# Kernel tuning notes

Measured on AMD Instinct MI355X. Metric: run time of the kernel, lower is better.

Reference implementation:

```python
import jax, jax.numpy as jnp
import numpy as np

B, CIN, C, H, W = 4, 256, 128, 64, 64
LN_EPS = 1e-5


def _conv1x1(x, Wk, bk):
    # x: [B, Cin, H, W], Wk: [Cout, Cin] -> [B, Cout, H, W]
    return jnp.einsum('bchw,oc->bohw', x, Wk) + bk[None, :, None, None]


def setup_inputs() -> dict:
    key = jax.random.key(0)
    ks = jax.random.split(key, 11)
    s_in = 1.0 / np.sqrt(CIN)
    s_c = 1.0 / np.sqrt(C)
    return {
        'x': jax.random.normal(ks[0], (B, CIN, H, W), jnp.float32),
        'Wg': jax.random.normal(ks[1], (C, CIN), jnp.float32) * s_in,
        'bg': jax.random.normal(ks[2], (C,), jnp.float32) * s_in,
        'Wt': jax.random.normal(ks[3], (C, CIN), jnp.float32) * s_in,
        'bt': jax.random.normal(ks[4], (C,), jnp.float32) * s_in,
        'Wp': jax.random.normal(ks[5], (C, CIN), jnp.float32) * s_in,
        'bp': jax.random.normal(ks[6], (C,), jnp.float32) * s_in,
        'Wz': jax.random.normal(ks[7], (CIN, C), jnp.float32) * s_c,
        'bz': jax.random.normal(ks[8], (CIN,), jnp.float32) * s_c,
        'gamma': jax.random.normal(ks[9], (CIN, H, W), jnp.float32),
        'beta': jax.random.normal(ks[10], (CIN,), jnp.float32).reshape(CIN, 1, 1) * jnp.ones((CIN, H, W), jnp.float32),
    }


def reference(x, Wg, bg, Wt, bt, Wp, bp, Wz, bz, gamma, beta):
    b, cin, h, w = x.shape
    n = h * w
    # 1x1 conv projections -> flatten spatial
    g = _conv1x1(x, Wg, bg).reshape(b, C, n).transpose(0, 2, 1)      # [B, N, C]
    theta = _conv1x1(x, Wt, bt).reshape(b, C, n).transpose(0, 2, 1)  # [B, N, C]
    phi = _conv1x1(x, Wp, bp).reshape(b, C, n)                        # [B, C, N]
    # embedded-gaussian attention: no scaling, softmax over keys
    f = jnp.einsum('bnc,bcm->bnm', theta, phi)                        # [B, N, N]
    attn = jax.nn.softmax(f, axis=-1)
    y = jnp.einsum('bnm,bmc->bnc', attn, g)                           # [B, N, C]
    y = y.transpose(0, 2, 1).reshape(b, C, h, w)                      # [B, C, H, W]
    # output projection + LayerNorm over [Cin, H, W]
    z = _conv1x1(y, Wz, bz)                                           # [B, Cin, H, W]
    mean = jnp.mean(z, axis=(1, 2, 3), keepdims=True)
    var = jnp.var(z, axis=(1, 2, 3), keepdims=True)
    ln = (z - mean) * jax.lax.rsqrt(var + LN_EPS) * gamma[None] + beta[None]
    return ln + x
```

## Files before the change

kernel.cpp:

```cpp
#include <hip/hip_runtime.h>
#include <hip/hip_bf16.h>


#define BB   4
#define CINC 256
#define CCH  128
#define NS   4096
#define LN_EPS 1e-5f

typedef unsigned short ushort_t;
typedef unsigned int   uint_t;
typedef __bf16 bf16x8 __attribute__((ext_vector_type(8)));
typedef float  f32x4  __attribute__((ext_vector_type(4)));
typedef float  f32x16 __attribute__((ext_vector_type(16)));

typedef const __attribute__((address_space(1))) void* gas_ptr;
typedef __attribute__((address_space(3))) void*       las_ptr;

__device__ __forceinline__ void gload16(const ushort_t* g, ushort_t* l) {
    __builtin_amdgcn_global_load_lds((gas_ptr)g, (las_ptr)l, 16, 0, 0);
}

__device__ __forceinline__ float4 ld4(const float* p) { return *reinterpret_cast<const float4*>(p); }
__device__ __forceinline__ void   st4(float* p, float4 v) { *reinterpret_cast<float4*>(p) = v; }

__device__ __forceinline__ ushort_t f2bf(float f) {
    __hip_bfloat16 h = __float2bfloat16(f);
    return *reinterpret_cast<ushort_t*>(&h);
}
__device__ __forceinline__ float bf2f(ushort_t u) {
    __hip_bfloat16 h = *reinterpret_cast<__hip_bfloat16*>(&u);
    return __bfloat162float(h);
}
__device__ __forceinline__ uint_t pk2(float a, float b) {
    return (uint_t)f2bf(a) | ((uint_t)f2bf(b) << 16);
}

__device__ __forceinline__ void split8(const float* v, uint_t* hw, uint_t* lw) {
#pragma unroll
    for (int jj = 0; jj < 4; ++jj) {
        ushort_t h0 = f2bf(v[2 * jj]);
        ushort_t h1 = f2bf(v[2 * jj + 1]);
        ushort_t e0 = f2bf(v[2 * jj] - bf2f(h0));
        ushort_t e1 = f2bf(v[2 * jj + 1] - bf2f(h1));
        hw[jj] = (uint_t)h0 | ((uint_t)h1 << 16);
        lw[jj] = (uint_t)e0 | ((uint_t)e1 << 16);
    }
}

__global__ __launch_bounds__(256) void split_kernel(
    const float* __restrict__ x,
    ushort_t* __restrict__ xTh, ushort_t* __restrict__ xTl)
{
    __shared__ float T[64 * 68];

    const int tid = threadIdx.x;
    const int n0  = blockIdx.x * 64;
    const int k0  = blockIdx.y * 64;
    const int b   = blockIdx.z;

#pragma unroll
    for (int u = 0; u < 4; ++u) {
        int fi = u * 256 + tid;
        int k  = fi >> 4;
        int c4 = fi & 15;
        float4 v = ld4(&x[(size_t)(b * CINC + k0 + k) * NS + n0 + c4 * 4]);
        T[(c4 * 4 + 0) * 68 + k] = v.x;
        T[(c4 * 4 + 1) * 68 + k] = v.y;
        T[(c4 * 4 + 2) * 68 + k] = v.z;
        T[(c4 * 4 + 3) * 68 + k] = v.w;
    }
    __syncthreads();

#pragma unroll
    for (int u = 0; u < 2; ++u) {
        int fi = u * 256 + tid;
        int n  = fi >> 3;
        int j  = fi & 7;
        float4 a0 = ld4(&T[n * 68 + j * 8]);
        float4 a1 = ld4(&T[n * 68 + j * 8 + 4]);
        float v[8] = {a0.x, a0.y, a0.z, a0.w, a1.x, a1.y, a1.z, a1.w};
        uint_t hw[4], lw[4];
        split8(v, hw, lw);
        size_t base = (size_t)(b * NS + n0 + n) * CINC + k0 + ((j ^ (n & 7)) * 8);
        *reinterpret_cast<uint4*>(&xTh[base]) = make_uint4(hw[0], hw[1], hw[2], hw[3]);
        *reinterpret_cast<uint4*>(&xTl[base]) = make_uint4(lw[0], lw[1], lw[2], lw[3]);
    }
}

__global__ __launch_bounds__(256) void wsplit_kernel(
    const float* __restrict__ Wt, const float* __restrict__ Wp,
    const float* __restrict__ Wg,
    ushort_t* __restrict__ Whs, ushort_t* __restrict__ Wls)
{
    int task = blockIdx.x * 256 + threadIdx.x;
    if (task >= 384 * 32) return;
    int o = task >> 5;
    int j = task & 31;
    int mid = o >> 7;
    int r   = o & 127;
    const float* Wsel = (mid == 0) ? Wt : (mid == 1) ? Wp : Wg;
    float4 a0 = ld4(&Wsel[(size_t)r * CINC + j * 8]);
    float4 a1 = ld4(&Wsel[(size_t)r * CINC + j * 8 + 4]);
    float v[8] = {a0.x, a0.y, a0.z, a0.w, a1.x, a1.y, a1.z, a1.w};
    uint_t hw[4], lw[4];
    split8(v, hw, lw);
    int kb = j >> 3, jj8 = j & 7;
    size_t base = (size_t)o * CINC + kb * 64 + ((jj8 ^ (o & 7)) * 8);
    *reinterpret_cast<uint4*>(&Whs[base]) = make_uint4(hw[0], hw[1], hw[2], hw[3]);
    *reinterpret_cast<uint4*>(&Wls[base]) = make_uint4(lw[0], lw[1], lw[2], lw[3]);
}

__global__ __launch_bounds__(256) void wsplitz_kernel(
    const float* __restrict__ Wz,
    ushort_t* __restrict__ Wzh, ushort_t* __restrict__ Wzl)
{
    int task = blockIdx.x * 256 + threadIdx.x;
    if (task >= 256 * 16) return;
    int o = task >> 4;
    int j = task & 15;
    float4 a0 = ld4(&Wz[(size_t)o * CCH + j * 8]);
    float4 a1 = ld4(&Wz[(size_t)o * CCH + j * 8 + 4]);
    float v[8] = {a0.x, a0.y, a0.z, a0.w, a1.x, a1.y, a1.z, a1.w};
    uint_t hw[4], lw[4];
    split8(v, hw, lw);
    size_t base = (size_t)o * CCH + (j >> 3) * 64 + (((j & 7) ^ (o & 7)) * 8);
    *reinterpret_cast<uint4*>(&Wzh[base]) = make_uint4(hw[0], hw[1], hw[2], hw[3]);
    *reinterpret_cast<uint4*>(&Wzl[base]) = make_uint4(lw[0], lw[1], lw[2], lw[3]);
}

__global__ __launch_bounds__(256) void proj_mfma_kernel(
    const ushort_t* __restrict__ xTh, const ushort_t* __restrict__ xTl,
    const ushort_t* __restrict__ Whs, const ushort_t* __restrict__ Wls,
    const float* __restrict__ bt, const float* __restrict__ bp,
    const float* __restrict__ bg,
    ushort_t* __restrict__ Qhi, ushort_t* __restrict__ Qlo,
    ushort_t* __restrict__ KhiS, ushort_t* __restrict__ KloS,
    ushort_t* __restrict__ VtS)
{
    __shared__ __align__(16) char smem[65536];
    ushort_t* Wh_l = (ushort_t*)smem;
    ushort_t* Wl_l = (ushort_t*)(smem + 16384);
    ushort_t* Xh_l = (ushort_t*)(smem + 32768);
    ushort_t* Xl_l = (ushort_t*)(smem + 49152);
    float*    T    = (float*)smem;

    const int tid  = threadIdx.x;
    const int w    = tid >> 6;
    const int lane = tid & 63;
    const int l31  = lane & 31;
    const int h    = lane >> 5;
    const int n0   = blockIdx.x * 128;
    const int og   = blockIdx.y;
    const int b    = blockIdx.z;

    const float* bsel = (og == 0) ? bt : (og == 1) ? bp : bg;

    f32x16 acc[4];
#pragma unroll
    for (int ng = 0; ng < 4; ++ng)
#pragma unroll
        for (int r = 0; r < 16; ++r) acc[ng][r] = 0.f;

    const int ol   = w * 32 + l31;
    const int swzq = l31 & 7;

    for (int kb = 0; kb < 4; ++kb) {
        if (kb > 0) __syncthreads();
#pragma unroll
        for (int p = 0; p < 4; ++p) {
            int e  = p * 2048 + tid * 8;
            int rr = e >> 6;
            int kk = e & 63;
            gload16(Whs + (size_t)(og * 128 + rr) * CINC + kb * 64 + kk, Wh_l + e);
            gload16(Wls + (size_t)(og * 128 + rr) * CINC + kb * 64 + kk, Wl_l + e);
            gload16(xTh + (size_t)(b * NS + n0 + rr) * CINC + kb * 64 + kk, Xh_l + e);
            gload16(xTl + (size_t)(b * NS + n0 + rr) * CINC + kb * 64 + kk, Xl_l + e);
        }
        __syncthreads();

        __builtin_amdgcn_s_setprio(1);
#pragma unroll
        for (int k16 = 0; k16 < 4; ++k16) {
            int c8  = k16 * 2 + h;
            int swz = c8 ^ swzq;
            bf16x8 ah = *reinterpret_cast<const bf16x8*>(&Wh_l[ol * 64 + swz * 8]);
            bf16x8 al = *reinterpret_cast<const bf16x8*>(&Wl_l[ol * 64 + swz * 8]);
#pragma unroll
            for (int ng = 0; ng < 4; ++ng) {
                int nl = ng * 32 + l31;
                bf16x8 xh = *reinterpret_cast<const bf16x8*>(&Xh_l[nl * 64 + swz * 8]);
                bf16x8 xl = *reinterpret_cast<const bf16x8*>(&Xl_l[nl * 64 + swz * 8]);
                acc[ng] = __builtin_amdgcn_mfma_f32_32x32x16_bf16(ah, xh, acc[ng], 0, 0, 0);
                acc[ng] = __builtin_amdgcn_mfma_f32_32x32x16_bf16(ah, xl, acc[ng], 0, 0, 0);
                acc[ng] = __builtin_amdgcn_mfma_f32_32x32x16_bf16(al, xh, acc[ng], 0, 0, 0);
            }
        }
        __builtin_amdgcn_s_setprio(0);
    }

    float bv[16];
#pragma unroll
    for (int r = 0; r < 16; ++r)
        bv[r] = bsel[w * 32 + (r & 3) + 8 * (r >> 2) + 4 * h];

    __syncthreads();

    if (og < 2) {
        ushort_t* H = (og == 0) ? Qhi : KhiS;
        ushort_t* L = (og == 0) ? Qlo : KloS;
#pragma unroll
        for (int pass = 0; pass < 2; ++pass) {
#pragma unroll
            for (int ngh = 0; ngh < 2; ++ngh) {
                int ng = pass * 2 + ngh;
                int nl = ngh * 32 + l31;
#pragma unroll
                for (int r = 0; r < 16; ++r) {
                    int o_in = w * 32 + (r & 3) + 8 * (r >> 2) + 4 * h;
                    T[nl * 132 + o_in] = acc[ng][r] + bv[r];
                }
            }
            __syncthreads();
#pragma unroll
            for (int u = 0; u < 4; ++u) {
                int fi = u * 256 + tid;
                int n  = fi >> 4;
                int j  = fi & 15;
                float4 a0 = ld4(&T[n * 132 + j * 8]);
                float4 a1 = ld4(&T[n * 132 + j * 8 + 4]);
                float v[8] = {a0.x, a0.y, a0.z, a0.w, a1.x, a1.y, a1.z, a1.w};
                uint_t hw[4], lw[4];
                split8(v, hw, lw);
                int n_glob = n0 + pass * 64 + n;
                int idx = (og == 1) ? ((j & 8) | ((j & 7) ^ (n & 7))) : j;
                size_t base = (size_t)(b * NS + n_glob) * CCH + idx * 8;
                *reinterpret_cast<uint4*>(&H[base]) = make_uint4(hw[0], hw[1], hw[2], hw[3]);
                *reinterpret_cast<uint4*>(&L[base]) = make_uint4(lw[0], lw[1], lw[2], lw[3]);
            }
            __syncthreads();
        }
    } else {
#pragma unroll
        for (int pass = 0; pass < 2; ++pass) {
            if ((w >> 1) == pass) {
#pragma unroll
                for (int ng = 0; ng < 4; ++ng) {
                    int nl = ng * 32 + l31;
#pragma unroll
                    for (int r = 0; r < 16; ++r) {
                        int c_loc = (w & 1) * 32 + (r & 3) + 8 * (r >> 2) + 4 * h;
                        T[c_loc * 132 + nl] = acc[ng][r] + bv[r];
                    }
                }
            }
            __syncthreads();
#pragma unroll
            for (int u = 0; u < 4; ++u) {
                int fi = u * 256 + tid;
                int c_loc = fi >> 4;
                int nj    = fi & 15;
                float4 a0 = ld4(&T[c_loc * 132 + nj * 8]);
                float4 a1 = ld4(&T[c_loc * 132 + nj * 8 + 4]);
                int c = pass * 64 + c_loc;
                uint4 wv;
                wv.x = pk2(a0.x, a0.y);
                wv.y = pk2(a0.z, a0.w);
                wv.z = pk2(a1.x, a1.y);
                wv.w = pk2(a1.z, a1.w);
                size_t base = (size_t)(b * CCH + c) * NS + n0 + (nj >> 3) * 64
                            + (((nj & 7) ^ (c & 7)) * 8);
                *reinterpret_cast<uint4*>(&VtS[base]) = wv;
            }
            __syncthreads();
        }
    }
}

__global__ __launch_bounds__(256, 2) void attn_kernel(
    const ushort_t* __restrict__ Qhi, const ushort_t* __restrict__ Qlo,
    const ushort_t* __restrict__ KhiS, const ushort_t* __restrict__ KloS,
    const ushort_t* __restrict__ VtS, float* __restrict__ Yp,
    float* __restrict__ ML, int NT)
{
    __shared__ __align__(16) char smem[81920];

    const int tid  = threadIdx.x;
    const int w    = tid >> 6;
    const int lane = tid & 63;
    const int l31  = lane & 31;
    const int h    = lane >> 5;

    int qx, sp, b;
    {
        int lin = (blockIdx.z * gridDim.y + blockIdx.y) * gridDim.x + blockIdx.x;
        if (gridDim.x * gridDim.y * gridDim.z == 512) {
            int xcd  = lin & 7;
            int idx  = lin >> 3;
            int pair = xcd * 2 + (idx >> 5);
            qx = idx & 31;
            b  = pair >> 2;
            sp = pair & 3;
        } else {
            qx = blockIdx.x;
            sp = blockIdx.y;
            b  = blockIdx.z;
        }
    }
    const int n0 = qx * 128;

    bf16x8 qh[8], ql[8];
    {
        const ushort_t* qrh = Qhi + (size_t)(b * NS + n0 + w * 32 + l31) * CCH;
        const ushort_t* qrl = Qlo + (size_t)(b * NS + n0 + w * 32 + l31) * CCH;
#pragma unroll
        for (int cst = 0; cst < 8; ++cst) {
            qh[cst] = *reinterpret_cast<const bf16x8*>(qrh + cst * 16 + h * 8);
            ql[cst] = *reinterpret_cast<const bf16x8*>(qrl + cst * 16 + h * 8);
        }
    }

    f32x16 yacc[4];
#pragma unroll
    for (int cb = 0; cb < 4; ++cb)
#pragma unroll
        for (int r = 0; r < 16; ++r) yacc[cb][r] = 0.f;
    float m_run = -1e30f, l_run = 0.f;

    const ushort_t* Khg = KhiS + (size_t)b * NS * CCH;
    const ushort_t* Klg = KloS + (size_t)b * NS * CCH;
    const ushort_t* Vtg = VtS + (size_t)b * CCH * NS;

    const int ktbase = sp * NT;

    auto gload_k = [&](int ktg, int bi) {
        ushort_t* kh = (ushort_t*)(smem + bi * 16384);
        ushort_t* kl = (ushort_t*)(smem + 32768 + bi * 16384);
        const size_t koff = (size_t)ktg * 8192;
#pragma unroll
        for (int i = 0; i < 4; ++i) {
            int off = i * 2048 + tid * 8;
            gload16(Khg + koff + off, kh + off);
            gload16(Klg + koff + off, kl + off);
        }
    };
    auto gload_v = [&](int ktg) {
        ushort_t* vb = (ushort_t*)(smem + 65536);
        const int m0 = ktg * 64;
#pragma unroll
        for (int i = 0; i < 4; ++i) {
            int off = i * 2048 + tid * 8;
            int cr = off >> 6;
            int cw = off & 63;
            gload16(Vtg + (size_t)cr * NS + m0 + cw, vb + off);
        }
    };

    gload_k(ktbase, 0);
    __syncthreads();

    const int swzq = l31 & 7;

    for (int kt = 0; kt < NT; ++kt) {
        const int cur = kt & 1;
        const bool more = (kt + 1 < NT);

        gload_v(ktbase + kt);
        if (more) gload_k(ktbase + kt + 1, cur ^ 1);

        const ushort_t* Kh = (const ushort_t*)(smem + cur * 16384);
        const ushort_t* Kl = (const ushort_t*)(smem + 32768 + cur * 16384);

        f32x16 sacc[2];
#pragma unroll
        for (int k2 = 0; k2 < 2; ++k2)
#pragma unroll
            for (int r = 0; r < 16; ++r) sacc[k2][r] = 0.f;

        __builtin_amdgcn_s_setprio(1);
#pragma unroll
        for (int cst = 0; cst < 8; ++cst) {
            int cc  = cst * 2 + h;
            int swz = (cc & 8) | ((cc & 7) ^ swzq);
#pragma unroll
            for (int k2 = 0; k2 < 2; ++k2) {
                int addr = (k2 * 32 + l31) * 128 + swz * 8;
                bf16x8 ah = *reinterpret_cast<const bf16x8*>(&Kh[addr]);
                bf16x8 al = *reinterpret_cast<const bf16x8*>(&Kl[addr]);
                sacc[k2] = __builtin_amdgcn_mfma_f32_32x32x16_bf16(ah, qh[cst], sacc[k2], 0, 0, 0);
                sacc[k2] = __builtin_amdgcn_mfma_f32_32x32x16_bf16(al, qh[cst], sacc[k2], 0, 0, 0);
                sacc[k2] = __builtin_amdgcn_mfma_f32_32x32x16_bf16(ah, ql[cst], sacc[k2], 0, 0, 0);
            }
        }
        __builtin_amdgcn_s_setprio(0);

        float mx = sacc[0][0];
#pragma unroll
        for (int r = 1; r < 16; ++r) mx = fmaxf(mx, sacc[0][r]);
#pragma unroll
        for (int r = 0; r < 16; ++r) mx = fmaxf(mx, sacc[1][r]);
        mx = fmaxf(mx, __shfl_xor(mx, 32));

        const bool defer = __all(mx - m_run <= 8.0f);
        float mref, alpha;
        if (defer) { mref = m_run; alpha = 1.0f; }
        else       { mref = fmaxf(m_run, mx); alpha = __expf(m_run - mref); }

        bf16x8 pb[4];
        float psum = 0.f;
#pragma unroll
        for (int k2 = 0; k2 < 2; ++k2) {
            float pe[16];
#pragma unroll
            for (int r = 0; r < 16; ++r) {
                pe[r] = __expf(sacc[k2][r] - mref);
                psum += pe[r];
            }
#pragma unroll
            for (int a = 0; a < 2; ++a) {
                uint_t w0 = pk2(pe[8 * a + 0], pe[8 * a + 1]);
                uint_t w1 = pk2(pe[8 * a + 2], pe[8 * a + 3]);
                uint_t w2 = pk2(pe[8 * a + 4], pe[8 * a + 5]);
                uint_t w3 = pk2(pe[8 * a + 6], pe[8 * a + 7]);
                uint_t s0 = (uint_t)__shfl_xor((int)w0, 32);
                uint_t s1 = (uint_t)__shfl_xor((int)w1, 32);
                uint_t s2 = (uint_t)__shfl_xor((int)w2, 32);
                uint_t s3 = (uint_t)__shfl_xor((int)w3, 32);
                uint_t u0 = h ? s2 : w0;
                uint_t u1 = h ? s3 : w1;
                uint_t u2 = h ? w2 : s0;
                uint_t u3 = h ? w3 : s1;
                uint4 packed = make_uint4(u0, u1, u2, u3);
                pb[k2 * 2 + a] = *reinterpret_cast<bf16x8*>(&packed);
            }
        }
        psum += __shfl_xor(psum, 32);

        if (more) {
            asm volatile("s_waitcnt vmcnt(8)" ::: "memory");
        } else {
            asm volatile("s_waitcnt vmcnt(0)" ::: "memory");
        }
        __builtin_amdgcn_s_barrier();
        __builtin_amdgcn_sched_barrier(0);

        if (defer) {
            l_run += psum;
        } else {
            l_run = l_run * alpha + psum;
            m_run = mref;
#pragma unroll
            for (int cb = 0; cb < 4; ++cb)
#pragma unroll
                for (int r = 0; r < 16; ++r) yacc[cb][r] *= alpha;
        }

        const ushort_t* Vl = (const ushort_t*)(smem + 65536);
        __builtin_amdgcn_s_setprio(1);
#pragma unroll
        for (int cb = 0; cb < 4; ++cb) {
            int crow = (cb * 32 + l31) * 64;
#pragma unroll
            for (int ks = 0; ks < 4; ++ks) {
                int kc = ks * 2 + h;
                bf16x8 av = *reinterpret_cast<const bf16x8*>(&Vl[crow + (kc ^ swzq) * 8]);
                yacc[cb] = __builtin_amdgcn_mfma_f32_32x32x16_bf16(av, pb[ks], yacc[cb], 0, 0, 0);
            }
        }
        __builtin_amdgcn_s_setprio(0);

        __syncthreads();
    }

    float* stage = (float*)smem;
    float* Ybase = Yp + ((size_t)(sp * BB + b) * NS + n0) * CCH;
#pragma unroll
    for (int pass = 0; pass < 2; ++pass) {
        if ((w >> 1) == pass) {
            int qrow = (w & 1) * 32 + l31;
#pragma unroll
            for (int cb = 0; cb < 4; ++cb)
#pragma unroll
                for (int r = 0; r < 16; ++r) {
                    int c = cb * 32 + (r & 3) + 8 * (r >> 2) + 4 * h;
                    stage[qrow * 132 + c] = yacc[cb][r];
                }
        }
        __syncthreads();
#pragma unroll
        for (int u = 0; u < 8; ++u) {
            int idx = u * 256 + tid;
            int row = idx >> 5;
            int c4  = idx & 31;
            st4(&Ybase[(size_t)(pass * 64 + row) * CCH + c4 * 4],
                ld4(&stage[row * 132 + c4 * 4]));
        }
        __syncthreads();
    }
    if (h == 0) {
        size_t mi = ((size_t)(sp * BB + b) * NS + n0 + w * 32 + l31) * 2;
        ML[mi + 0] = m_run;
        ML[mi + 1] = l_run;
    }
}

__global__ __launch_bounds__(256) void merge_kernel(
    const float* __restrict__ Yp, const float* __restrict__ ML,
    ushort_t* __restrict__ Ymh, ushort_t* __restrict__ Yml, int nsplit)
{
    const int total = BB * NS * (CCH / 8);
    for (int t = blockIdx.x * 256 + threadIdx.x; t < total;
         t += gridDim.x * 256) {
        int b = t >> 16;
        int r = t & 65535;
        int n = r >> 4;
        int j = r & 15;

        float ms[4], ls[4];
        float m = -1e30f;
#pragma unroll
        for (int s = 0; s < 4; ++s) {
            if (s < nsplit) {
                size_t mi = ((size_t)(s * BB + b) * NS + n) * 2;
                ms[s] = ML[mi + 0];
                ls[s] = ML[mi + 1];
                m = fmaxf(m, ms[s]);
            }
        }
        float den = 0.f;
        float wt[4];
#pragma unroll
        for (int s = 0; s < 4; ++s) {
            if (s < nsplit) {
                wt[s] = __expf(ms[s] - m);
                den += ls[s] * wt[s];
            }
        }
        float inv = 1.0f / den;

        float acc[8] = {0.f, 0.f, 0.f, 0.f, 0.f, 0.f, 0.f, 0.f};
#pragma unroll
        for (int s = 0; s < 4; ++s) {
            if (s < nsplit) {
                float a = wt[s] * inv;
                const float* yr = &Yp[((size_t)(s * BB + b) * NS + n) * CCH + j * 8];
                float4 y0 = ld4(yr);
                float4 y1 = ld4(yr + 4);
                acc[0] += a * y0.x; acc[1] += a * y0.y;
                acc[2] += a * y0.z; acc[3] += a * y0.w;
                acc[4] += a * y1.x; acc[5] += a * y1.y;
                acc[6] += a * y1.z; acc[7] += a * y1.w;
            }
        }
        uint_t hw[4], lw[4];
        split8(acc, hw, lw);
        size_t base = (size_t)(b * NS + n) * CCH + (j >> 3) * 64
                    + (((j & 7) ^ (n & 7)) * 8);
        *reinterpret_cast<uint4*>(&Ymh[base]) = make_uint4(hw[0], hw[1], hw[2], hw[3]);
        *reinterpret_cast<uint4*>(&Yml[base]) = make_uint4(lw[0], lw[1], lw[2], lw[3]);
    }
}

__global__ __launch_bounds__(256) void zgemm_kernel(
    const ushort_t* __restrict__ Ymh, const ushort_t* __restrict__ Yml,
    const ushort_t* __restrict__ Wzh, const ushort_t* __restrict__ Wzl,
    const float* __restrict__ bz, float* __restrict__ Z,
    float* __restrict__ partials)
{
    __shared__ __align__(16) char smem[65536];
    ushort_t* Wh_l = (ushort_t*)smem;
    ushort_t* Wl_l = (ushort_t*)(smem + 16384);
    ushort_t* Yh_l = (ushort_t*)(smem + 32768);
    ushort_t* Yl_l = (ushort_t*)(smem + 49152);
    __shared__ float red[8];

    const int tid  = threadIdx.x;
    const int w    = tid >> 6;
    const int lane = tid & 63;
    const int l31  = lane & 31;
    const int h    = lane >> 5;
    const int n0   = blockIdx.x * 128;
    const int o0   = blockIdx.y * 128;
    const int b    = blockIdx.z;

    f32x16 acc[4];
#pragma unroll
    for (int ng = 0; ng < 4; ++ng)
#pragma unroll
        for (int r = 0; r < 16; ++r) acc[ng][r] = 0.f;

    const int ol   = w * 32 + l31;
    const int swzq = l31 & 7;

    for (int kb = 0; kb < 2; ++kb) {
        if (kb > 0) __syncthreads();
#pragma unroll
        for (int p = 0; p < 4; ++p) {
            int e  = p * 2048 + tid * 8;
            int rr = e >> 6;
            int kk = e & 63;
            gload16(Wzh + (size_t)(o0 + rr) * CCH + kb * 64 + kk, Wh_l + e);
            gload16(Wzl + (size_t)(o0 + rr) * CCH + kb * 64 + kk, Wl_l + e);
            gload16(Ymh + (size_t)(b * NS + n0 + rr) * CCH + kb * 64 + kk, Yh_l + e);
            gload16(Yml + (size_t)(b * NS + n0 + rr) * CCH + kb * 64 + kk, Yl_l + e);
        }
        __syncthreads();

        __builtin_amdgcn_s_setprio(1);
#pragma unroll
        for (int k16 = 0; k16 < 4; ++k16) {
            int c8  = k16 * 2 + h;
            int swz = c8 ^ swzq;
            bf16x8 ah = *reinterpret_cast<const bf16x8*>(&Wh_l[ol * 64 + swz * 8]);
            bf16x8 al = *reinterpret_cast<const bf16x8*>(&Wl_l[ol * 64 + swz * 8]);
#pragma unroll
            for (int ng = 0; ng < 4; ++ng) {
                int nl = ng * 32 + l31;
                bf16x8 yh = *reinterpret_cast<const bf16x8*>(&Yh_l[nl * 64 + swz * 8]);
                bf16x8 yl = *reinterpret_cast<const bf16x8*>(&Yl_l[nl * 64 + swz * 8]);
                acc[ng] = __builtin_amdgcn_mfma_f32_32x32x16_bf16(ah, yh, acc[ng], 0, 0, 0);
                acc[ng] = __builtin_amdgcn_mfma_f32_32x32x16_bf16(ah, yl, acc[ng], 0, 0, 0);
                acc[ng] = __builtin_amdgcn_mfma_f32_32x32x16_bf16(al, yh, acc[ng], 0, 0, 0);
            }
        }
        __builtin_amdgcn_s_setprio(0);
    }

    float s = 0.f, s2 = 0.f;
#pragma unroll
    for (int r = 0; r < 16; ++r) {
        int o = o0 + w * 32 + (r & 3) + 8 * (r >> 2) + 4 * h;
        float bias = bz[o];
        float* zrow = &Z[(size_t)(b * CINC + o) * NS + n0 + l31];
#pragma unroll
        for (int ng = 0; ng < 4; ++ng) {
            float v = acc[ng][r] + bias;
            zrow[ng * 32] = v;
            s  += v;
            s2 += v * v;
        }
    }
#pragma unroll
    for (int off = 1; off < 64; off <<= 1) {
        s  += __shfl_xor(s, off);
        s2 += __shfl_xor(s2, off);
    }
    if (lane == 0) { red[w * 2] = s; red[w * 2 + 1] = s2; }
    __syncthreads();
    if (tid == 0) {
        float ts  = red[0] + red[2] + red[4] + red[6];
        float ts2 = red[1] + red[3] + red[5] + red[7];
        int pidx = (b * 2 + blockIdx.y) * 32 + blockIdx.x;
        partials[pidx * 2 + 0] = ts;
        partials[pidx * 2 + 1] = ts2;
    }
}

__global__ void ln_stats_kernel(const float* __restrict__ partials,
                                float* __restrict__ stats)
{
    const int b = blockIdx.x;
    const int t = threadIdx.x;
    float s  = partials[(size_t)(b * 64 + t) * 2 + 0];
    float s2 = partials[(size_t)(b * 64 + t) * 2 + 1];
#pragma unroll
    for (int off = 1; off < 64; off <<= 1) {
        s  += __shfl_xor(s, off);
        s2 += __shfl_xor(s2, off);
    }
    if (t == 0) {
        const float M = 1048576.f;
        float mean = s / M;
        float var  = s2 / M - mean * mean;
        stats[b * 2 + 0] = mean;
        stats[b * 2 + 1] = rsqrtf(var + LN_EPS);
    }
}

__global__ __launch_bounds__(256) void final_kernel(
    const float* __restrict__ Z, const float* __restrict__ x,
    const float* __restrict__ gamma, const float* __restrict__ beta,
    const float* __restrict__ stats, float* __restrict__ out)
{
    const int total4 = BB * CINC * NS / 4;
    for (int i4 = blockIdx.x * 256 + threadIdx.x; i4 < total4;
         i4 += gridDim.x * 256) {
        int b  = i4 >> 18;
        int r4 = i4 & ((1 << 18) - 1);
        float mean = stats[b * 2 + 0];
        float rstd = stats[b * 2 + 1];
        float4 zv = ld4(&Z[(size_t)i4 * 4]);
        float4 xv = ld4(&x[(size_t)i4 * 4]);
        float4 gv = ld4(&gamma[(size_t)r4 * 4]);
        float4 bv = ld4(&beta[(size_t)r4 * 4]);
        float4 o;
        o.x = (zv.x - mean) * rstd * gv.x + bv.x + xv.x;
        o.y = (zv.y - mean) * rstd * gv.y + bv.y + xv.y;
        o.z = (zv.z - mean) * rstd * gv.z + bv.z + xv.z;
        o.w = (zv.w - mean) * rstd * gv.w + bv.w + xv.w;
        st4(&out[(size_t)i4 * 4], o);
    }
}

extern "C" void kernel_launch(void* const* d_in, const int* in_sizes, int n_in,
                              void* d_out, int out_size, void* d_ws, size_t ws_size,
                              hipStream_t stream)
{
    const float* x     = (const float*)d_in[0];
    const float* Wg    = (const float*)d_in[1];
    const float* bg    = (const float*)d_in[2];
    const float* Wt    = (const float*)d_in[3];
    const float* bt    = (const float*)d_in[4];
    const float* Wp    = (const float*)d_in[5];
    const float* bp    = (const float*)d_in[6];
    const float* Wz    = (const float*)d_in[7];
    const float* bz    = (const float*)d_in[8];
    const float* gamma = (const float*)d_in[9];
    const float* beta  = (const float*)d_in[10];
    float* out = (float*)d_out;

    const size_t SZH = (size_t)BB * NS * CCH * sizeof(ushort_t);
    const size_t need4 = 5 * SZH
                       + (size_t)4 * BB * NS * CCH * sizeof(float)
                       + (size_t)4 * BB * NS * 2 * sizeof(float)
                       + (size_t)BB * 64 * 2 * sizeof(float) + 256;
    const int nsplit = (ws_size >= need4) ? 4 : 2;
    const int NT = (NS / 64) / nsplit;

    char* p = (char*)d_ws;
    ushort_t* Qhi  = (ushort_t*)p; p += SZH;
    ushort_t* Qlo  = (ushort_t*)p; p += SZH;
    ushort_t* KhiS = (ushort_t*)p; p += SZH;
    ushort_t* KloS = (ushort_t*)p; p += SZH;
    ushort_t* VtS  = (ushort_t*)p; p += SZH;
    float* Yp = (float*)p; p += (size_t)nsplit * BB * NS * CCH * sizeof(float);
    float* ML = (float*)p; p += (size_t)nsplit * BB * NS * 2 * sizeof(float);
    float* partials = (float*)p; p += BB * 64 * 2 * sizeof(float);
    float* stats    = (float*)p;

    ushort_t* Ymh = (ushort_t*)Qhi;
    ushort_t* Yml = (ushort_t*)Qlo;
    ushort_t* Wzh = (ushort_t*)KhiS;
    ushort_t* Wzl = (ushort_t*)KloS;
    float*    Z   = (float*)Yp;

    ushort_t* xTh = (ushort_t*)Yp;
    ushort_t* xTl = xTh + (size_t)BB * NS * CINC;
    ushort_t* Whs = (ushort_t*)((char*)Yp + 2 * (size_t)BB * NS * CINC * 2);
    ushort_t* Wls = Whs + (size_t)384 * CINC;

    split_kernel<<<dim3(NS / 64, CINC / 64, BB), 256, 0, stream>>>(x, xTh, xTl);
    wsplit_kernel<<<dim3(48), 256, 0, stream>>>(Wt, Wp, Wg, Whs, Wls);
    proj_mfma_kernel<<<dim3(NS / 128, 3, BB), 256, 0, stream>>>(
        xTh, xTl, Whs, Wls, bt, bp, bg, Qhi, Qlo, KhiS, KloS, VtS);
    attn_kernel<<<dim3(NS / 128, nsplit, BB), 256, 0, stream>>>(
        Qhi, Qlo, KhiS, KloS, VtS, Yp, ML, NT);
    wsplitz_kernel<<<dim3(16), 256, 0, stream>>>(Wz, Wzh, Wzl);
    merge_kernel<<<dim3(1024), 256, 0, stream>>>(Yp, ML, Ymh, Yml, nsplit);
    zgemm_kernel<<<dim3(NS / 128, 2, BB), 256, 0, stream>>>(
        Ymh, Yml, Wzh, Wzl, bz, Z, partials);
    ln_stats_kernel<<<dim3(BB), 64, 0, stream>>>(partials, stats);
    final_kernel<<<dim3(2048), 256, 0, stream>>>(Z, x, gamma, beta, stats, out);
}
```

Baseline: 135.7 us.

## Software-pipeline attention loop with 32-key tiles, overlapping QK of next tile with PV

Shrinks the key tile from 64 to 32 keys and restructures the attention loop so the QK^T MFMAs for tile kt run alongside softmax and PV for tile kt-1. V is now double-buffered with K, and the V transposed layout swizzle is changed to match 32-wide rows. LDS use drops from 80KB to 48KB, which may allow more resident blocks, but the loop runs twice as many iterations with extra barriers and finer-grained waits.

```diff
diff --git a/kernel.cpp b/kernel.cpp
--- a/kernel.cpp
+++ b/kernel.cpp
@@ -268,8 +268,8 @@
                 wv.y = pk2(a0.z, a0.w);
                 wv.z = pk2(a1.x, a1.y);
                 wv.w = pk2(a1.z, a1.w);
-                size_t base = (size_t)(b * CCH + c) * NS + n0 + (nj >> 3) * 64
-                            + (((nj & 7) ^ (c & 7)) * 8);
+                size_t base = (size_t)(b * CCH + c) * NS + n0 + (nj >> 2) * 32
+                            + (((nj & 3) ^ (c & 3)) * 8);
                 *reinterpret_cast<uint4*>(&VtS[base]) = wv;
             }
             __syncthreads();
@@ -283,7 +283,7 @@
     const ushort_t* __restrict__ VtS, float* __restrict__ Yp,
     float* __restrict__ ML, int NT)
 {
-    __shared__ __align__(16) char smem[81920];
+    __shared__ __align__(16) char smem[49152];
 
     const int tid  = threadIdx.x;
     const int w    = tid >> 6;
@@ -302,9 +302,7 @@
             b  = pair >> 2;
             sp = pair & 3;
         } else {
-            qx = blockIdx.x;
-            sp = blockIdx.y;
-            b  = blockIdx.z;
+            qx = blockIdx.x; sp = blockIdx.y; b = blockIdx.z;
         }
     }
     const int n0 = qx * 128;
@@ -326,124 +324,89 @@
 #pragma unroll
         for (int r = 0; r < 16; ++r) yacc[cb][r] = 0.f;
     float m_run = -1e30f, l_run = 0.f;
+    f32x16 sC, sP;
+    bf16x8 pb[2];
 
     const ushort_t* Khg = KhiS + (size_t)b * NS * CCH;
     const ushort_t* Klg = KloS + (size_t)b * NS * CCH;
     const ushort_t* Vtg = VtS + (size_t)b * CCH * NS;
 
     const int ktbase = sp * NT;
+    const int swzq = l31 & 7;
+    const int swzv = l31 & 3;
 
     auto gload_k = [&](int ktg, int bi) {
-        ushort_t* kh = (ushort_t*)(smem + bi * 16384);
-        ushort_t* kl = (ushort_t*)(smem + 32768 + bi * 16384);
-        const size_t koff = (size_t)ktg * 8192;
-#pragma unroll
-        for (int i = 0; i < 4; ++i) {
+        ushort_t* kh = (ushort_t*)(smem + bi * 8192);
+        ushort_t* kl = (ushort_t*)(smem + 16384 + bi * 8192);
+        const size_t koff = (size_t)ktg * 4096;
+#pragma unroll
+        for (int i = 0; i < 2; ++i) {
             int off = i * 2048 + tid * 8;
             gload16(Khg + koff + off, kh + off);
             gload16(Klg + koff + off, kl + off);
         }
     };
-    auto gload_v = [&](int ktg) {
-        ushort_t* vb = (ushort_t*)(smem + 65536);
-        const int m0 = ktg * 64;
-#pragma unroll
-        for (int i = 0; i < 4; ++i) {
+    auto gload_v = [&](int ktg, int bi) {
+        ushort_t* vb = (ushort_t*)(smem + 32768 + bi * 8192);
+        const int m0 = ktg * 32;
+#pragma unroll
+        for (int i = 0; i < 2; ++i) {
             int off = i * 2048 + tid * 8;
-            int cr = off >> 6;
-            int cw = off & 63;
+            int cr = off >> 5;
+            int cw = off & 31;
             gload16(Vtg + (size_t)cr * NS + m0 + cw, vb + off);
         }
     };
 
-    gload_k(ktbase, 0);
-    __syncthreads();
-
-    const int swzq = l31 & 7;
-
-    for (int kt = 0; kt < NT; ++kt) {
-        const int cur = kt & 1;
-        const bool more = (kt + 1 < NT);
-
-        gload_v(ktbase + kt);
-        if (more) gload_k(ktbase + kt + 1, cur ^ 1);
-
-        const ushort_t* Kh = (const ushort_t*)(smem + cur * 16384);
-        const ushort_t* Kl = (const ushort_t*)(smem + 32768 + cur * 16384);
-
-        f32x16 sacc[2];
-#pragma unroll
-        for (int k2 = 0; k2 < 2; ++k2)
-#pragma unroll
-            for (int r = 0; r < 16; ++r) sacc[k2][r] = 0.f;
-
+    auto qk = [&](int bi, f32x16& s) {
+        const ushort_t* Kh = (const ushort_t*)(smem + bi * 8192);
+        const ushort_t* Kl = (const ushort_t*)(smem + 16384 + bi * 8192);
         __builtin_amdgcn_s_setprio(1);
 #pragma unroll
         for (int cst = 0; cst < 8; ++cst) {
             int cc  = cst * 2 + h;
             int swz = (cc & 8) | ((cc & 7) ^ swzq);
-#pragma unroll
-            for (int k2 = 0; k2 < 2; ++k2) {
-                int addr = (k2 * 32 + l31) * 128 + swz * 8;
-                bf16x8 ah = *reinterpret_cast<const bf16x8*>(&Kh[addr]);
-                bf16x8 al = *reinterpret_cast<const bf16x8*>(&Kl[addr]);
-                sacc[k2] = __builtin_amdgcn_mfma_f32_32x32x16_bf16(ah, qh[cst], sacc[k2], 0, 0, 0);
-                sacc[k2] = __builtin_amdgcn_mfma_f32_32x32x16_bf16(al, qh[cst], sacc[k2], 0, 0, 0);
-                sacc[k2] = __builtin_amdgcn_mfma_f32_32x32x16_bf16(ah, ql[cst], sacc[k2], 0, 0, 0);
-            }
+            int addr = l31 * 128 + swz * 8;
+            bf16x8 ah = *reinterpret_cast<const bf16x8*>(&Kh[addr]);
+            bf16x8 al = *reinterpret_cast<const bf16x8*>(&Kl[addr]);
+            s = __builtin_amdgcn_mfma_f32_32x32x16_bf16(ah, qh[cst], s, 0, 0, 0);
+            s = __builtin_amdgcn_mfma_f32_32x32x16_bf16(al, qh[cst], s, 0, 0, 0);
+            s = __builtin_amdgcn_mfma_f32_32x32x16_bf16(ah, ql[cst], s, 0, 0, 0);
         }
         __builtin_amdgcn_s_setprio(0);
-
-        float mx = sacc[0][0];
-#pragma unroll
-        for (int r = 1; r < 16; ++r) mx = fmaxf(mx, sacc[0][r]);
-#pragma unroll
-        for (int r = 0; r < 16; ++r) mx = fmaxf(mx, sacc[1][r]);
+    };
+
+    auto softmax_pack = [&](f32x16& s) {
+        float mx = s[0];
+#pragma unroll
+        for (int r = 1; r < 16; ++r) mx = fmaxf(mx, s[r]);
         mx = fmaxf(mx, __shfl_xor(mx, 32));
-
         const bool defer = __all(mx - m_run <= 8.0f);
         float mref, alpha;
         if (defer) { mref = m_run; alpha = 1.0f; }
         else       { mref = fmaxf(m_run, mx); alpha = __expf(m_run - mref); }
-
-        bf16x8 pb[4];
         float psum = 0.f;
 #pragma unroll
-        for (int k2 = 0; k2 < 2; ++k2) {
-            float pe[16];
-#pragma unroll
-            for (int r = 0; r < 16; ++r) {
-                pe[r] = __expf(sacc[k2][r] - mref);
-                psum += pe[r];
-            }
-#pragma unroll
-            for (int a = 0; a < 2; ++a) {
-                uint_t w0 = pk2(pe[8 * a + 0], pe[8 * a + 1]);
-                uint_t w1 = pk2(pe[8 * a + 2], pe[8 * a + 3]);
-                uint_t w2 = pk2(pe[8 * a + 4], pe[8 * a + 5]);
-                uint_t w3 = pk2(pe[8 * a + 6], pe[8 * a + 7]);
-                uint_t s0 = (uint_t)__shfl_xor((int)w0, 32);
-                uint_t s1 = (uint_t)__shfl_xor((int)w1, 32);
-                uint_t s2 = (uint_t)__shfl_xor((int)w2, 32);
-                uint_t s3 = (uint_t)__shfl_xor((int)w3, 32);
-                uint_t u0 = h ? s2 : w0;
-                uint_t u1 = h ? s3 : w1;
-                uint_t u2 = h ? w2 : s0;
-                uint_t u3 = h ? w3 : s1;
-                uint4 packed = make_uint4(u0, u1, u2, u3);
-                pb[k2 * 2 + a] = *reinterpret_cast<bf16x8*>(&packed);
-            }
+        for (int r = 0; r < 16; ++r) {
+            float v = __expf(s[r] - mref);
+            s[r] = v;
+            psum += v;
+        }
+#pragma unroll
+        for (int a = 0; a < 2; ++a) {
+            uint_t w0 = pk2(s[8 * a + 0], s[8 * a + 1]);
+            uint_t w1 = pk2(s[8 * a + 2], s[8 * a + 3]);
+            uint_t w2 = pk2(s[8 * a + 4], s[8 * a + 5]);
+            uint_t w3 = pk2(s[8 * a + 6], s[8 * a + 7]);
+            uint_t s0 = (uint_t)__shfl_xor((int)w0, 32);
+            uint_t s1 = (uint_t)__shfl_xor((int)w1, 32);
+            uint_t s2 = (uint_t)__shfl_xor((int)w2, 32);
+            uint_t s3 = (uint_t)__shfl_xor((int)w3, 32);
+            uint4 packed = make_uint4(h ? s2 : w0, h ? s3 : w1,
+                                      h ? w2 : s0, h ? w3 : s1);
+            pb[a] = *reinterpret_cast<bf16x8*>(&packed);
         }
         psum += __shfl_xor(psum, 32);
-
-        if (more) {
-            asm volatile("s_waitcnt vmcnt(8)" ::: "memory");
-        } else {
-            asm volatile("s_waitcnt vmcnt(0)" ::: "memory");
-        }
-        __builtin_amdgcn_s_barrier();
-        __builtin_amdgcn_sched_barrier(0);
-
         if (defer) {
             l_run += psum;
         } else {
@@ -454,23 +417,65 @@
 #pragma unroll
                 for (int r = 0; r < 16; ++r) yacc[cb][r] *= alpha;
         }
-
-        const ushort_t* Vl = (const ushort_t*)(smem + 65536);
+    };
+
+    auto pv = [&](int bi) {
+        const ushort_t* Vl = (const ushort_t*)(smem + 32768 + bi * 8192);
         __builtin_amdgcn_s_setprio(1);
 #pragma unroll
         for (int cb = 0; cb < 4; ++cb) {
-            int crow = (cb * 32 + l31) * 64;
-#pragma unroll
-            for (int ks = 0; ks < 4; ++ks) {
+            int crow = (cb * 32 + l31) * 32;
+#pragma unroll
+            for (int ks = 0; ks < 2; ++ks) {
                 int kc = ks * 2 + h;
-                bf16x8 av = *reinterpret_cast<const bf16x8*>(&Vl[crow + (kc ^ swzq) * 8]);
+                bf16x8 av = *reinterpret_cast<const bf16x8*>(&Vl[crow + (kc ^ swzv) * 8]);
                 yacc[cb] = __builtin_amdgcn_mfma_f32_32x32x16_bf16(av, pb[ks], yacc[cb], 0, 0, 0);
             }
         }
         __builtin_amdgcn_s_setprio(0);
-
-        __syncthreads();
-    }
+    };
+
+    gload_k(ktbase, 0);
+    __syncthreads();
+    gload_k(ktbase + 1, 1);
+    gload_v(ktbase, 0);
+#pragma unroll
+    for (int r = 0; r < 16; ++r) sC[r] = 0.f;
+    qk(0, sC);
+    asm volatile("s_waitcnt vmcnt(2)\ns_barrier" ::: "memory");
+    __builtin_amdgcn_sched_barrier(0);
+    sP = sC;
+
+    for (int kt = 1; kt < NT; ++kt) {
+        const int cur = kt & 1;
+        if (kt + 1 < NT) gload_k(ktbase + kt + 1, cur ^ 1);
+        gload_v(ktbase + kt, cur);
+
+#pragma unroll
+        for (int r = 0; r < 16; ++r) sC[r] = 0.f;
+        qk(cur, sC);
+        softmax_pack(sP);
+
+        if (kt + 1 < NT)
+            asm volatile("s_waitcnt vmcnt(6)\ns_barrier" ::: "memory");
+        else
+            asm volatile("s_waitcnt vmcnt(2)\ns_barrier" ::: "memory");
+        __builtin_amdgcn_sched_barrier(0);
+
+        pv((kt - 1) & 1);
+
+        if (kt + 1 < NT) {
+            asm volatile("s_waitcnt vmcnt(2)\ns_barrier" ::: "memory");
+            __builtin_amdgcn_sched_barrier(0);
+        }
+        sP = sC;
+    }
+
+    softmax_pack(sP);
+    asm volatile("s_waitcnt vmcnt(0)\ns_barrier" ::: "memory");
+    __builtin_amdgcn_sched_barrier(0);
+    pv((NT - 1) & 1);
+    __syncthreads();
 
     float* stage = (float*)smem;
     float* Ybase = Yp + ((size_t)(sp * BB + b) * NS + n0) * CCH;
@@ -725,7 +730,7 @@
                        + (size_t)4 * BB * NS * 2 * sizeof(float)
                        + (size_t)BB * 64 * 2 * sizeof(float) + 256;
     const int nsplit = (ws_size >= need4) ? 4 : 2;
-    const int NT = (NS / 64) / nsplit;
+    const int NT = (NS / 32) / nsplit;
 
     char* p = (char*)d_ws;
     ushort_t* Qhi  = (ushort_t*)p; p += SZH;
```

Result: slower. 140.3 us (+3.4%).

## Drop K double-buffering in attention to fit three blocks per CU; merge weight-split kernels

Applied to the files above, without the earlier changes.

The attention kernel's shared memory goes from 80KB to 48KB by removing the double-buffered K tile and the overlapped async loads. Each K/V tile is now loaded synchronously after compute, and launch bounds are raised to 3 blocks per CU so other resident blocks can hide the latency. The two weight-split kernels are merged into one launch, with Wz's split copy given its own workspace slot so it can be produced early. The trade is losing intra-block load/compute overlap in exchange for higher occupancy, which also puts tighter register limits on the attention kernel.

```diff
diff --git a/kernel.cpp b/kernel.cpp
--- a/kernel.cpp
+++ b/kernel.cpp
@@ -88,45 +88,41 @@
     }
 }
 
-__global__ __launch_bounds__(256) void wsplit_kernel(
+__global__ __launch_bounds__(256) void wsplit_all_kernel(
     const float* __restrict__ Wt, const float* __restrict__ Wp,
-    const float* __restrict__ Wg,
-    ushort_t* __restrict__ Whs, ushort_t* __restrict__ Wls)
+    const float* __restrict__ Wg, const float* __restrict__ Wz,
+    ushort_t* __restrict__ Whs, ushort_t* __restrict__ Wls,
+    ushort_t* __restrict__ Wzh, ushort_t* __restrict__ Wzl)
 {
     int task = blockIdx.x * 256 + threadIdx.x;
-    if (task >= 384 * 32) return;
-    int o = task >> 5;
-    int j = task & 31;
-    int mid = o >> 7;
-    int r   = o & 127;
-    const float* Wsel = (mid == 0) ? Wt : (mid == 1) ? Wp : Wg;
-    float4 a0 = ld4(&Wsel[(size_t)r * CINC + j * 8]);
-    float4 a1 = ld4(&Wsel[(size_t)r * CINC + j * 8 + 4]);
-    float v[8] = {a0.x, a0.y, a0.z, a0.w, a1.x, a1.y, a1.z, a1.w};
-    uint_t hw[4], lw[4];
-    split8(v, hw, lw);
-    int kb = j >> 3, jj8 = j & 7;
-    size_t base = (size_t)o * CINC + kb * 64 + ((jj8 ^ (o & 7)) * 8);
-    *reinterpret_cast<uint4*>(&Whs[base]) = make_uint4(hw[0], hw[1], hw[2], hw[3]);
-    *reinterpret_cast<uint4*>(&Wls[base]) = make_uint4(lw[0], lw[1], lw[2], lw[3]);
-}
-
-__global__ __launch_bounds__(256) void wsplitz_kernel(
-    const float* __restrict__ Wz,
-    ushort_t* __restrict__ Wzh, ushort_t* __restrict__ Wzl)
-{
-    int task = blockIdx.x * 256 + threadIdx.x;
-    if (task >= 256 * 16) return;
-    int o = task >> 4;
-    int j = task & 15;
-    float4 a0 = ld4(&Wz[(size_t)o * CCH + j * 8]);
-    float4 a1 = ld4(&Wz[(size_t)o * CCH + j * 8 + 4]);
-    float v[8] = {a0.x, a0.y, a0.z, a0.w, a1.x, a1.y, a1.z, a1.w};
-    uint_t hw[4], lw[4];
-    split8(v, hw, lw);
-    size_t base = (size_t)o * CCH + (j >> 3) * 64 + (((j & 7) ^ (o & 7)) * 8);
-    *reinterpret_cast<uint4*>(&Wzh[base]) = make_uint4(hw[0], hw[1], hw[2], hw[3]);
-    *reinterpret_cast<uint4*>(&Wzl[base]) = make_uint4(lw[0], lw[1], lw[2], lw[3]);
+    if (task < 384 * 32) {
+        int o = task >> 5;
+        int j = task & 31;
+        int mid = o >> 7;
+        int r   = o & 127;
+        const float* Wsel = (mid == 0) ? Wt : (mid == 1) ? Wp : Wg;
+        float4 a0 = ld4(&Wsel[(size_t)r * CINC + j * 8]);
+        float4 a1 = ld4(&Wsel[(size_t)r * CINC + j * 8 + 4]);
+        float v[8] = {a0.x, a0.y, a0.z, a0.w, a1.x, a1.y, a1.z, a1.w};
+        uint_t hw[4], lw[4];
+        split8(v, hw, lw);
+        int kb = j >> 3, jj8 = j & 7;
+        size_t base = (size_t)o * CINC + kb * 64 + ((jj8 ^ (o & 7)) * 8);
+        *reinterpret_cast<uint4*>(&Whs[base]) = make_uint4(hw[0], hw[1], hw[2], hw[3]);
+        *reinterpret_cast<uint4*>(&Wls[base]) = make_uint4(lw[0], lw[1], lw[2], lw[3]);
+    } else {
+        int t2 = task - 384 * 32;
+        int o = t2 >> 4;
+        int j = t2 & 15;
+        float4 a0 = ld4(&Wz[(size_t)o * CCH + j * 8]);
+        float4 a1 = ld4(&Wz[(size_t)o * CCH + j * 8 + 4]);
+        float v[8] = {a0.x, a0.y, a0.z, a0.w, a1.x, a1.y, a1.z, a1.w};
+        uint_t hw[4], lw[4];
+        split8(v, hw, lw);
+        size_t base = (size_t)o * CCH + (j >> 3) * 64 + (((j & 7) ^ (o & 7)) * 8);
+        *reinterpret_cast<uint4*>(&Wzh[base]) = make_uint4(hw[0], hw[1], hw[2], hw[3]);
+        *reinterpret_cast<uint4*>(&Wzl[base]) = make_uint4(lw[0], lw[1], lw[2], lw[3]);
+    }
 }
 
 __global__ __launch_bounds__(256) void proj_mfma_kernel(
@@ -277,13 +273,13 @@
     }
 }
 
-__global__ __launch_bounds__(256, 2) void attn_kernel(
+__global__ __launch_bounds__(256, 3) void attn_kernel(
     const ushort_t* __restrict__ Qhi, const ushort_t* __restrict__ Qlo,
     const ushort_t* __restrict__ KhiS, const ushort_t* __restrict__ KloS,
     const ushort_t* __restrict__ VtS, float* __restrict__ Yp,
     float* __restrict__ ML, int NT)
 {
-    __shared__ __align__(16) char smem[81920];
+    __shared__ __align__(16) char smem[49152];
 
     const int tid  = threadIdx.x;
     const int w    = tid >> 6;
@@ -302,9 +298,7 @@
             b  = pair >> 2;
             sp = pair & 3;
         } else {
-            qx = blockIdx.x;
-            sp = blockIdx.y;
-            b  = blockIdx.z;
+            qx = blockIdx.x; sp = blockIdx.y; b = blockIdx.z;
         }
     }
     const int n0 = qx * 128;
@@ -332,45 +326,30 @@
     const ushort_t* Vtg = VtS + (size_t)b * CCH * NS;
 
     const int ktbase = sp * NT;
-
-    auto gload_k = [&](int ktg, int bi) {
-        ushort_t* kh = (ushort_t*)(smem + bi * 16384);
-        ushort_t* kl = (ushort_t*)(smem + 32768 + bi * 16384);
+    const int swzq = l31 & 7;
+
+    ushort_t* KhL = (ushort_t*)smem;
+    ushort_t* KlL = (ushort_t*)(smem + 16384);
+    ushort_t* VL  = (ushort_t*)(smem + 32768);
+
+    auto gload_tile = [&](int ktg) {
         const size_t koff = (size_t)ktg * 8192;
+        const int m0 = ktg * 64;
 #pragma unroll
         for (int i = 0; i < 4; ++i) {
             int off = i * 2048 + tid * 8;
-            gload16(Khg + koff + off, kh + off);
-            gload16(Klg + koff + off, kl + off);
-        }
-    };
-    auto gload_v = [&](int ktg) {
-        ushort_t* vb = (ushort_t*)(smem + 65536);
-        const int m0 = ktg * 64;
-#pragma unroll
-        for (int i = 0; i < 4; ++i) {
-            int off = i * 2048 + tid * 8;
+            gload16(Khg + koff + off, KhL + off);
+            gload16(Klg + koff + off, KlL + off);
             int cr = off >> 6;
             int cw = off & 63;
-            gload16(Vtg + (size_t)cr * NS + m0 + cw, vb + off);
+            gload16(Vtg + (size_t)cr * NS + m0 + cw, VL + off);
         }
     };
 
-    gload_k(ktbase, 0);
+    gload_tile(ktbase);
     __syncthreads();
 
-    const int swzq = l31 & 7;
-
     for (int kt = 0; kt < NT; ++kt) {
-        const int cur = kt & 1;
-        const bool more = (kt + 1 < NT);
-
-        gload_v(ktbase + kt);
-        if (more) gload_k(ktbase + kt + 1, cur ^ 1);
-
-        const ushort_t* Kh = (const ushort_t*)(smem + cur * 16384);
-        const ushort_t* Kl = (const ushort_t*)(smem + 32768 + cur * 16384);
-
         f32x16 sacc[2];
 #pragma unroll
         for (int k2 = 0; k2 < 2; ++k2)
@@ -385,8 +364,8 @@
 #pragma unroll
             for (int k2 = 0; k2 < 2; ++k2) {
                 int addr = (k2 * 32 + l31) * 128 + swz * 8;
-                bf16x8 ah = *reinterpret_cast<const bf16x8*>(&Kh[addr]);
-                bf16x8 al = *reinterpret_cast<const bf16x8*>(&Kl[addr]);
+                bf16x8 ah = *reinterpret_cast<const bf16x8*>(&KhL[addr]);
+                bf16x8 al = *reinterpret_cast<const bf16x8*>(&KlL[addr]);
                 sacc[k2] = __builtin_amdgcn_mfma_f32_32x32x16_bf16(ah, qh[cst], sacc[k2], 0, 0, 0);
                 sacc[k2] = __builtin_amdgcn_mfma_f32_32x32x16_bf16(al, qh[cst], sacc[k2], 0, 0, 0);
                 sacc[k2] = __builtin_amdgcn_mfma_f32_32x32x16_bf16(ah, ql[cst], sacc[k2], 0, 0, 0);
@@ -436,14 +415,6 @@
         }
         psum += __shfl_xor(psum, 32);
 
-        if (more) {
-            asm volatile("s_waitcnt vmcnt(8)" ::: "memory");
-        } else {
-            asm volatile("s_waitcnt vmcnt(0)" ::: "memory");
-        }
-        __builtin_amdgcn_s_barrier();
-        __builtin_amdgcn_sched_barrier(0);
-
         if (defer) {
             l_run += psum;
         } else {
@@ -455,7 +426,6 @@
                 for (int r = 0; r < 16; ++r) yacc[cb][r] *= alpha;
         }
 
-        const ushort_t* Vl = (const ushort_t*)(smem + 65536);
         __builtin_amdgcn_s_setprio(1);
 #pragma unroll
         for (int cb = 0; cb < 4; ++cb) {
@@ -463,13 +433,17 @@
 #pragma unroll
             for (int ks = 0; ks < 4; ++ks) {
                 int kc = ks * 2 + h;
-                bf16x8 av = *reinterpret_cast<const bf16x8*>(&Vl[crow + (kc ^ swzq) * 8]);
+                bf16x8 av = *reinterpret_cast<const bf16x8*>(&VL[crow + (kc ^ swzq) * 8]);
                 yacc[cb] = __builtin_amdgcn_mfma_f32_32x32x16_bf16(av, pb[ks], yacc[cb], 0, 0, 0);
             }
         }
         __builtin_amdgcn_s_setprio(0);
 
         __syncthreads();
+        if (kt + 1 < NT) {
+            gload_tile(ktbase + kt + 1);
+            __syncthreads();
+        }
     }
 
     float* stage = (float*)smem;
@@ -720,10 +694,12 @@
     float* out = (float*)d_out;
 
     const size_t SZH = (size_t)BB * NS * CCH * sizeof(ushort_t);
+    const size_t WZB = (size_t)CINC * CCH * sizeof(ushort_t);
     const size_t need4 = 5 * SZH
                        + (size_t)4 * BB * NS * CCH * sizeof(float)
                        + (size_t)4 * BB * NS * 2 * sizeof(float)
-                       + (size_t)BB * 64 * 2 * sizeof(float) + 256;
+                       + (size_t)BB * 64 * 2 * sizeof(float)
+                       + 2 * WZB + 512;
     const int nsplit = (ws_size >= need4) ? 4 : 2;
     const int NT = (NS / 64) / nsplit;
 
@@ -736,12 +712,12 @@
     float* Yp = (float*)p; p += (size_t)nsplit * BB * NS * CCH * sizeof(float);
     float* ML = (float*)p; p += (size_t)nsplit * BB * NS * 2 * sizeof(float);
     float* partials = (float*)p; p += BB * 64 * 2 * sizeof(float);
-    float* stats    = (float*)p;
+    float* stats    = (float*)p; p += 64;
+    ushort_t* Wzh = (ushort_t*)p; p += WZB;
+    ushort_t* Wzl = (ushort_t*)p;
 
     ushort_t* Ymh = (ushort_t*)Qhi;
     ushort_t* Yml = (ushort_t*)Qlo;
-    ushort_t* Wzh = (ushort_t*)KhiS;
-    ushort_t* Wzl = (ushort_t*)KloS;
     float*    Z   = (float*)Yp;
 
     ushort_t* xTh = (ushort_t*)Yp;
@@ -750,12 +726,12 @@
     ushort_t* Wls = Whs + (size_t)384 * CINC;
 
     split_kernel<<<dim3(NS / 64, CINC / 64, BB), 256, 0, stream>>>(x, xTh, xTl);
-    wsplit_kernel<<<dim3(48), 256, 0, stream>>>(Wt, Wp, Wg, Whs, Wls);
+    wsplit_all_kernel<<<dim3(64), 256, 0, stream>>>(Wt, Wp, Wg, Wz,
+                                                    Whs, Wls, Wzh, Wzl);
     proj_mfma_kernel<<<dim3(NS / 128, 3, BB), 256, 0, stream>>>(
         xTh, xTl, Whs, Wls, bt, bp, bg, Qhi, Qlo, KhiS, KloS, VtS);
     attn_kernel<<<dim3(NS / 128, nsplit, BB), 256, 0, stream>>>(
         Qhi, Qlo, KhiS, KloS, VtS, Yp, ML, NT);
-    wsplitz_kernel<<<dim3(16), 256, 0, stream>>>(Wz, Wzh, Wzl);
     merge_kernel<<<dim3(1024), 256, 0, stream>>>(Yp, ML, Ymh, Yml, nsplit);
     zgemm_kernel<<<dim3(NS / 128, 2, BB), 256, 0, stream>>>(
         Ymh, Yml, Wzh, Wzl, bz, Z, partials);
```

New measurement: 167.2 us. +23.2%, slower.
